# Performance work log

Measured on AMD Instinct MI355X. Metric: run time of the kernel, lower is better.

Reference implementation:

```python
import jax, jax.numpy as jnp
import numpy as np

B, L, E, D = 32, 1024, 512, 512  # batch, seq_len, input_size, per-direction hidden
SCALE = 1.4142135623730951  # rescale=True, highway_bias=0 -> sqrt(1+exp(0*2)) = sqrt(2)


def setup_inputs() -> dict:
    key = jax.random.key(0)
    ks = jax.random.split(key, 12)
    g = lambda k, shape, s: (jax.random.normal(k, shape, jnp.float32) * s)
    return {
        "seqs": jax.random.normal(ks[0], (B, L, E), jnp.float32),
        # layer 0: input E -> 2 dirs * 4 projections * D
        "W0": g(ks[1], (E, 8 * D), (1.0 / E) ** 0.5),
        "vf0": g(ks[2], (2, D), 0.1), "vr0": g(ks[3], (2, D), 0.1),
        "bf0": jnp.zeros((2, D), jnp.float32), "br0": jnp.zeros((2, D), jnp.float32),
        # layer 1: input 2D -> 2 dirs * 4 projections * D
        "W1": g(ks[4], (2 * D, 8 * D), (1.0 / (2 * D)) ** 0.5),
        "vf1": g(ks[5], (2, D), 0.1), "vr1": g(ks[6], (2, D), 0.1),
        "bf1": jnp.zeros((2, D), jnp.float32), "br1": jnp.zeros((2, D), jnp.float32),
        "lengths": jax.random.randint(ks[7], (B,), 1, L + 1, dtype=jnp.int32),
    }


def _sru_dir(u, vf, vr, bf, br, reverse):
    # u: (L, B, 4, D) -> h: (L, B, D), c_T: (B, D)
    def step(c, u_t):
        xt, fp, rp, xp = u_t[:, 0], u_t[:, 1], u_t[:, 2], u_t[:, 3]
        f = jax.nn.sigmoid(fp + vf * c + bf)
        c_new = f * c + (1.0 - f) * xt
        r = jax.nn.sigmoid(rp + vr * c + br)
        h = r * c_new + (1.0 - r) * xp * SCALE
        return c_new, h

    c0 = jnp.zeros((u.shape[1], u.shape[-1]), u.dtype)
    cT, hs = jax.lax.scan(step, c0, u, reverse=reverse)
    return hs, cT


def _sru_layer(x, W, vf, vr, bf, br):
    # x: (L, B, n_in)
    Lx, Bx = x.shape[0], x.shape[1]
    U = (x @ W).reshape(Lx, Bx, 2, 4, -1)  # dirs, (x_tilde, f, r, x_resid)
    h_f, c_f = _sru_dir(U[:, :, 0], vf[0], vr[0], bf[0], br[0], False)
    h_b, c_b = _sru_dir(U[:, :, 1], vf[1], vr[1], bf[1], br[1], True)
    return jnp.concatenate([h_f, h_b], -1), jnp.concatenate([c_f, c_b], -1)


def reference(seqs, W0, vf0, vr0, bf0, br0, W1, vf1, vr1, bf1, br1, lengths):
    x = jnp.transpose(seqs, (1, 0, 2))  # (L, B, E)
    out0, _ = _sru_layer(x, W0, vf0, vr0, bf0, br0)
    out1, c1 = _sru_layer(out0, W1, vf1, vr1, bf1, br1)
    # module returns (h[1], output.transpose(0,1)): layer-1 final cell state, (B,L,2D) outputs
    return c1, jnp.transpose(out1, (1, 0, 2))
```

## Files before the change

kernel.cpp:

```cpp
#include <hip/hip_runtime.h>
#include <cstdint>
#include <cstddef>

#define B_   32
#define L_   1024
#define D_   512
#define M_   (B_ * L_)
#define N8D  4096
#define SCALEF 1.4142135623730951f
#define LOG2E 1.4426950408889634f

typedef unsigned short u16;
typedef __bf16 bf16x8 __attribute__((ext_vector_type(8)));
typedef unsigned short u16x8 __attribute__((ext_vector_type(8)));
typedef unsigned short u16x4 __attribute__((ext_vector_type(4)));
typedef float f32x4 __attribute__((ext_vector_type(4)));

__device__ __forceinline__ float bf2f(u16 u) {
    union { unsigned int i; float f; } v; v.i = ((unsigned int)u) << 16; return v.f;
}
__device__ __forceinline__ u16 f2bf(float x) {
    union { float f; unsigned int i; } v; v.f = x;
    unsigned int r = (v.i + 0x7fffu + ((v.i >> 16) & 1u)) >> 16;
    return (u16)r;
}
__device__ __forceinline__ float sigmoid_fast(float z) {
    return __builtin_amdgcn_rcpf(1.0f + __builtin_amdgcn_exp2f(-LOG2E * z));
}

__device__ __forceinline__ void gl2lds16(const u16* g, u16* l) {
    __builtin_amdgcn_global_load_lds(
        (const __attribute__((address_space(1))) void*)g,
        (__attribute__((address_space(3))) void*)l, 16, 0, 0);
}

#define VMW(n) asm volatile("s_waitcnt vmcnt(" #n ")" ::: "memory")

__global__ __launch_bounds__(256) void f32_to_bf16(const float* __restrict__ in,
                                                   u16* __restrict__ out) {
    size_t i = ((size_t)blockIdx.x * 256 + threadIdx.x) * 8;
    f32x4 v0 = *(const f32x4*)(in + i);
    f32x4 v1 = *(const f32x4*)(in + i + 4);
    u16x8 o;
#pragma unroll
    for (int q = 0; q < 4; ++q) { o[q] = f2bf(v0[q]); o[4 + q] = f2bf(v1[q]); }
    *(u16x8*)(out + i) = o;
}

__global__ __launch_bounds__(256) void transpose_w(const float* __restrict__ in,
                                                   u16* __restrict__ out,
                                                   int R, int C) {
    __shared__ u16 tile[32][33];
    int bx = blockIdx.x * 32;
    int by = blockIdx.y * 32;
    int tx = threadIdx.x & 31;
    int ty = threadIdx.x >> 5;
#pragma unroll
    for (int i = 0; i < 32; i += 8)
        tile[ty + i][tx] = f2bf(in[(size_t)(by + ty + i) * C + bx + tx]);
    __syncthreads();
#pragma unroll
    for (int i = 0; i < 32; i += 8) {
        int n = bx + ty + i;
        int p = (n >> 11) * 2048 + ((n & 511) << 2) + ((n >> 9) & 3);
        out[(size_t)p * R + by + tx] = tile[tx][ty + i];
    }
}

__global__ __launch_bounds__(512, 2) void gemm256(const u16* __restrict__ A,
                                                  const u16* __restrict__ BT,
                                                  u16* __restrict__ U, int K) {
    extern __shared__ __align__(16) u16 lds[];
    const int t    = threadIdx.x;
    const int lane = t & 63;
    const int wave = t >> 6;
    const int wm   = wave >> 2;
    const int wn   = wave & 3;
    const int qm   = lane & 15;
    const int quad = lane >> 4;

    const int nwg = gridDim.x;
    const int wg  = blockIdx.x;
    const int swz = (wg & 7) * (nwg >> 3) + (wg >> 3);
    const int bn  = (swz & 15) << 8;
    const int bm  = (swz >> 4) << 8;

    const int P0   = t * 16;
    const int L0   = P0 ^ ((P0 >> 3) & 0x30);
    const int srow = L0 >> 6;
    const int scol = (L0 & 63) >> 1;
    const u16* Ag = A  + (size_t)(bm + srow) * K + scol;
    const u16* Bg = BT + (size_t)(bn + srow) * K + scol;
    const size_t g128 = (size_t)128 * K;
    u16* ldst = lds + t * 8;

    const int fxor  = (quad * 16) ^ ((qm & 6) << 3);
    const int aBase = (wm * 128 + qm) * 64 + fxor;
    const int bBase = (wn * 64  + qm) * 64 + fxor;
    const char* ldsc = (const char*)lds;

    f32x4 acc[8][4];
#pragma unroll
    for (int i = 0; i < 8; ++i)
#pragma unroll
        for (int j = 0; j < 4; ++j) acc[i][j] = (f32x4)(0.0f);

    bf16x8 aA[4], aB[4];
    bf16x8 bK0[4], bK1[4];

#define STG(op, tile, ks, buf) do {                                          \
        const u16* g_ = ((op) ? Bg : Ag) + (size_t)(tile) * 64 + (ks) * 32;  \
        u16* l_ = ldst + (buf) * 32768 + (op) * 16384 + (ks) * 8192;         \
        gl2lds16(g_, l_);                                                    \
        gl2lds16(g_ + g128, l_ + 4096);                                      \
    } while (0)

#define RD_A(dst, buf, ks, mh) do {                                          \
        _Pragma("unroll")                                                    \
        for (int mi = 0; mi < 4; ++mi)                                       \
            dst[mi] = *(const bf16x8*)(ldsc + ((buf) * 65536 + (ks) * 16384) \
                          + aBase + ((mh) * 64 + mi * 16) * 64);             \
    } while (0)

#define RD_B(dst, buf, ks) do {                                              \
        _Pragma("unroll")                                                    \
        for (int nj = 0; nj < 4; ++nj)                                       \
            dst[nj] = *(const bf16x8*)(ldsc + ((buf) * 65536 + 32768 +       \
                          (ks) * 16384) + bBase + nj * 16 * 64);             \
    } while (0)

#define MFMA16(mh, AU, BU) do {                                              \
        __builtin_amdgcn_s_barrier();                                        \
        asm volatile("s_waitcnt lgkmcnt(0)" ::: "memory");                   \
        __builtin_amdgcn_sched_barrier(0);                                   \
        __builtin_amdgcn_s_setprio(1);                                       \
        _Pragma("unroll")                                                    \
        for (int mi = 0; mi < 4; ++mi)                                       \
            _Pragma("unroll")                                                \
            for (int nj = 0; nj < 4; ++nj)                                   \
                acc[(mh) * 4 + mi][nj] = __builtin_amdgcn_mfma_f32_16x16x32_bf16( \
                    AU[mi], BU[nj], acc[(mh) * 4 + mi][nj], 0, 0, 0);        \
        __builtin_amdgcn_s_setprio(0);                                       \
    } while (0)

#define BARB __builtin_amdgcn_s_barrier()

    const int nt = K >> 6;

    STG(1, 0, 0, 0); STG(0, 0, 0, 0); STG(1, 0, 1, 0); STG(0, 0, 1, 0);
    VMW(4);
    STG(1, 1, 0, 1); STG(0, 1, 0, 1); STG(1, 1, 1, 1);
    VMW(6);
    __builtin_amdgcn_s_barrier();
    RD_A(aA, 0, 0, 0); RD_B(bK0, 0, 0);

    const int niter = (nt >> 1) - 1;
    for (int i = 0; i < niter; ++i) {
        const int tp1 = 2 * i + 1, tp2 = 2 * i + 2, tp3 = 2 * i + 3;
        STG(0, tp1, 1, 1); MFMA16(0, aA, bK0); RD_A(aB, 0, 0, 1); BARB;
        STG(1, tp2, 0, 0); MFMA16(1, aB, bK0); RD_A(aA, 0, 1, 0); RD_B(bK1, 0, 1); BARB;
        STG(0, tp2, 0, 0); MFMA16(0, aA, bK1); RD_A(aB, 0, 1, 1); BARB;
        STG(1, tp2, 1, 0); MFMA16(1, aB, bK1); VMW(6); RD_A(aA, 1, 0, 0); RD_B(bK0, 1, 0); BARB;
        STG(0, tp2, 1, 0); MFMA16(0, aA, bK0); RD_A(aB, 1, 0, 1); BARB;
        STG(1, tp3, 0, 1); MFMA16(1, aB, bK0); RD_A(aA, 1, 1, 0); RD_B(bK1, 1, 1); BARB;
        STG(0, tp3, 0, 1); MFMA16(0, aA, bK1); RD_A(aB, 1, 1, 1); BARB;
        STG(1, tp3, 1, 1); MFMA16(1, aB, bK1); VMW(6); RD_A(aA, 0, 0, 0); RD_B(bK0, 0, 0); BARB;
    }
    STG(0, nt - 1, 1, 1); MFMA16(0, aA, bK0); RD_A(aB, 0, 0, 1); BARB;
    MFMA16(1, aB, bK0); RD_A(aA, 0, 1, 0); RD_B(bK1, 0, 1); BARB;
    MFMA16(0, aA, bK1); RD_A(aB, 0, 1, 1); BARB;
    MFMA16(1, aB, bK1); VMW(4); RD_A(aA, 1, 0, 0); RD_B(bK0, 1, 0); BARB;
    MFMA16(0, aA, bK0); RD_A(aB, 1, 0, 1); BARB;
    MFMA16(1, aB, bK0); VMW(0); RD_A(aA, 1, 1, 0); RD_B(bK1, 1, 1); BARB;
    MFMA16(0, aA, bK1); RD_A(aB, 1, 1, 1); BARB;
    MFMA16(1, aB, bK1); BARB;

#undef BARB
#undef MFMA16
#undef RD_B
#undef RD_A
#undef STG

#pragma unroll
    for (int i8 = 0; i8 < 8; ++i8) {
        const int row0 = bm + wm * 128 + (i8 >> 2) * 64 + (i8 & 3) * 16 + quad * 4;
#pragma unroll
        for (int nj = 0; nj < 4; ++nj) {
            const int col = bn + wn * 64 + nj * 16 + qm;
#pragma unroll
            for (int r = 0; r < 4; ++r)
                U[(size_t)(row0 + r) * N8D + col] = f2bf(acc[i8][nj][r]);
        }
    }
}

template<bool OUT_F32>
__global__ __launch_bounds__(64) void sru_scan(const u16* __restrict__ U,
                                               const float* __restrict__ vf,
                                               const float* __restrict__ vr,
                                               const float* __restrict__ bfv,
                                               const float* __restrict__ brv,
                                               void* __restrict__ Hv,
                                               void* __restrict__ Cv) {
    constexpr int PF = 32;
    constexpr int NB = L_ / PF;

    int gid = blockIdx.x * blockDim.x + threadIdx.x;
    int d   = gid & (D_ - 1);
    int dir = (gid >> 9) & 1;
    int b   = gid >> 10;
    int ch  = dir * D_ + d;

    const float vf_v = vf[ch];
    const float vr_v = vr[ch];
    const float bf_v = bfv[ch];
    const float br_v = brv[ch];

    const ptrdiff_t ustep = dir ? -(ptrdiff_t)N8D : (ptrdiff_t)N8D;
    const ptrdiff_t hstep = dir ? -(ptrdiff_t)1024 : (ptrdiff_t)1024;
    const u16* p0 = U + (size_t)b * L_ * N8D + dir * 2048 + d * 4
                      + (dir ? (size_t)(L_ - 1) * N8D : 0);
    const size_t hstart = (size_t)b * L_ * 1024 + ch + (dir ? (size_t)(L_ - 1) * 1024 : 0);
    float* Hf = (float*)Hv + hstart;
    u16*   Hh = (u16*)Hv + hstart;

    float c = 0.0f;

    auto loadB = [&](u16x4 (&buf)[PF], int tb) {
        const u16* base = p0 + (ptrdiff_t)tb * PF * ustep;
#pragma unroll
        for (int i = 0; i < PF; ++i)
            buf[i] = *(const u16x4*)(base + (ptrdiff_t)i * ustep);
    };
    auto compStore = [&](u16x4 (&buf)[PF], int tb) {
        const ptrdiff_t hb = (ptrdiff_t)tb * PF * hstep;
#pragma unroll
        for (int i = 0; i < PF; ++i) {
            float xt = bf2f(buf[i][0]), fp = bf2f(buf[i][1]);
            float rp = bf2f(buf[i][2]), xp = bf2f(buf[i][3]);
            float f = sigmoid_fast(fp + vf_v * c + bf_v);
            float r = sigmoid_fast(rp + vr_v * c + br_v);
            c = f * (c - xt) + xt;
            float xs = xp * SCALEF;
            float h  = r * (c - xs) + xs;
            ptrdiff_t ho = hb + (ptrdiff_t)i * hstep;
            if (OUT_F32) Hf[ho] = h; else Hh[ho] = f2bf(h);
        }
    };

    u16x4 b0[PF], b1[PF];
    loadB(b0, 0);
    loadB(b1, 1);
    for (int t = 0; t < NB; t += 2) {
        compStore(b0, t);
        if (t + 2 < NB) loadB(b0, t + 2);
        compStore(b1, t + 1);
        if (t + 3 < NB) loadB(b1, t + 3);
    }

    if (OUT_F32) ((float*)Cv)[b * 1024 + ch] = c;
    else         ((u16*)Cv)[b * 1024 + ch]  = f2bf(c);
}

extern "C" void kernel_launch(void* const* d_in, const int* in_sizes, int n_in,
                              void* d_out, int out_size, void* d_ws, size_t ws_size,
                              hipStream_t stream) {
    (void)in_sizes; (void)n_in; (void)out_size; (void)ws_size;

    const float* seqs = (const float*)d_in[0];
    const float* W0   = (const float*)d_in[1];
    const float* vf0  = (const float*)d_in[2];
    const float* vr0  = (const float*)d_in[3];
    const float* bf0  = (const float*)d_in[4];
    const float* br0  = (const float*)d_in[5];
    const float* W1   = (const float*)d_in[6];
    const float* vf1  = (const float*)d_in[7];
    const float* vr1  = (const float*)d_in[8];
    const float* bf1  = (const float*)d_in[9];
    const float* br1  = (const float*)d_in[10];

    float* out = (float*)d_out;
    char* ws = (char*)d_ws;

    const size_t U_BYTES  = (size_t)M_ * N8D * 2;
    const size_t H_BYTES  = (size_t)M_ * 1024 * 2;
    const size_t W0T_B    = (size_t)4096 * 512 * 2;
    const size_t W1T_B    = (size_t)4096 * 1024 * 2;

    u16* U   = (u16*)(ws);
    u16* H0  = (u16*)(ws + U_BYTES);
    u16* S16 = H0;
    u16* W0T = (u16*)(ws + U_BYTES + H_BYTES);
    u16* W1T = (u16*)(ws + U_BYTES + H_BYTES + W0T_B);
    u16* Cd  = (u16*)(ws + U_BYTES + H_BYTES + W0T_B + W1T_B);

    f32_to_bf16<<<dim3(M_ * 512 / 8 / 256), 256, 0, stream>>>(seqs, S16);

    transpose_w<<<dim3(4096 / 32, 512 / 32), 256, 0, stream>>>(W0, W0T, 512, 4096);
    transpose_w<<<dim3(4096 / 32, 1024 / 32), 256, 0, stream>>>(W1, W1T, 1024, 4096);

    gemm256<<<dim3(2048), 512, 131072, stream>>>(S16, W0T, U, 512);
    sru_scan<false><<<dim3(512), 64, 0, stream>>>(U, vf0, vr0, bf0, br0, (void*)H0, (void*)Cd);

    gemm256<<<dim3(2048), 512, 131072, stream>>>(H0, W1T, U, 1024);
    sru_scan<true><<<dim3(512), 64, 0, stream>>>(U, vf1, vr1, bf1, br1,
                                                 (void*)(out + B_ * 1024), (void*)out);
}
```

Baseline: 774.5 us.

## Restructure GEMM main loop into per-k-slice phases with interleaved LDS waits

```diff
diff --git a/kernel.cpp b/kernel.cpp
--- a/kernel.cpp
+++ b/kernel.cpp
@@ -35,6 +35,8 @@
 }
 
 #define VMW(n) asm volatile("s_waitcnt vmcnt(" #n ")" ::: "memory")
+#define LGK(n) asm volatile("s_waitcnt lgkmcnt(" #n ")" ::: "memory")
+#define SB     __builtin_amdgcn_sched_barrier(0)
 
 __global__ __launch_bounds__(256) void f32_to_bf16(const float* __restrict__ in,
                                                    u16* __restrict__ out) {
@@ -105,81 +107,76 @@
 #pragma unroll
         for (int j = 0; j < 4; ++j) acc[i][j] = (f32x4)(0.0f);
 
-    bf16x8 aA[4], aB[4];
-    bf16x8 bK0[4], bK1[4];
-
-#define STG(op, tile, ks, buf) do {                                          \
+#define RD16(p) (*(const bf16x8*)(p))
+
+#define STGR(op, tile, ks, buf) do {                                         \
         const u16* g_ = ((op) ? Bg : Ag) + (size_t)(tile) * 64 + (ks) * 32;  \
         u16* l_ = ldst + (buf) * 32768 + (op) * 16384 + (ks) * 8192;         \
         gl2lds16(g_, l_);                                                    \
         gl2lds16(g_ + g128, l_ + 4096);                                      \
     } while (0)
 
-#define RD_A(dst, buf, ks, mh) do {                                          \
-        _Pragma("unroll")                                                    \
-        for (int mi = 0; mi < 4; ++mi)                                       \
-            dst[mi] = *(const bf16x8*)(ldsc + ((buf) * 65536 + (ks) * 16384) \
-                          + aBase + ((mh) * 64 + mi * 16) * 64);             \
-    } while (0)
-
-#define RD_B(dst, buf, ks) do {                                              \
+#define G4(g, av) do {                                                       \
         _Pragma("unroll")                                                    \
         for (int nj = 0; nj < 4; ++nj)                                       \
-            dst[nj] = *(const bf16x8*)(ldsc + ((buf) * 65536 + 32768 +       \
-                          (ks) * 16384) + bBase + nj * 16 * 64);             \
+            acc[g][nj] = __builtin_amdgcn_mfma_f32_16x16x32_bf16(            \
+                av, bb[nj], acc[g][nj], 0, 0, 0);                            \
     } while (0)
 
-#define MFMA16(mh, AU, BU) do {                                              \
-        __builtin_amdgcn_s_barrier();                                        \
-        asm volatile("s_waitcnt lgkmcnt(0)" ::: "memory");                   \
-        __builtin_amdgcn_sched_barrier(0);                                   \
+#define PH(buf, ks, stile, dostage, vmn, dobar) do {                         \
+        const char* As_ = ldsc + ((buf) * 32768 + (ks) * 8192) * 2;          \
+        const char* Bs_ = ldsc + ((buf) * 32768 + 16384 + (ks) * 8192) * 2;  \
+        bf16x8 bb[4], aa[8];                                                 \
+        bb[0] = RD16(Bs_ + bBase);        SB;                                \
+        bb[1] = RD16(Bs_ + bBase + 1024); SB;                                \
+        bb[2] = RD16(Bs_ + bBase + 2048); SB;                                \
+        bb[3] = RD16(Bs_ + bBase + 3072); SB;                                \
+        aa[0] = RD16(As_ + aBase);        SB;                                \
+        aa[1] = RD16(As_ + aBase + 1024); SB;                                \
+        aa[2] = RD16(As_ + aBase + 2048); SB;                                \
+        aa[3] = RD16(As_ + aBase + 3072); SB;                                \
+        aa[4] = RD16(As_ + aBase + 4096); SB;                                \
+        aa[5] = RD16(As_ + aBase + 5120); SB;                                \
+        aa[6] = RD16(As_ + aBase + 6144); SB;                                \
+        aa[7] = RD16(As_ + aBase + 7168); SB;                                \
+        if (dostage) { STGR(0, stile, ks, (buf) ^ 1);                        \
+                       STGR(1, stile, ks, (buf) ^ 1); }                      \
         __builtin_amdgcn_s_setprio(1);                                       \
-        _Pragma("unroll")                                                    \
-        for (int mi = 0; mi < 4; ++mi)                                       \
-            _Pragma("unroll")                                                \
-            for (int nj = 0; nj < 4; ++nj)                                   \
-                acc[(mh) * 4 + mi][nj] = __builtin_amdgcn_mfma_f32_16x16x32_bf16( \
-                    AU[mi], BU[nj], acc[(mh) * 4 + mi][nj], 0, 0, 0);        \
+        LGK(7); SB; G4(0, aa[0]); SB;                                        \
+        LGK(6); SB; G4(1, aa[1]); SB;                                        \
+        LGK(5); SB; G4(2, aa[2]); SB;                                        \
+        LGK(4); SB; G4(3, aa[3]); SB;                                        \
+        LGK(3); SB; G4(4, aa[4]); SB;                                        \
+        LGK(2); SB; G4(5, aa[5]); SB;                                        \
+        LGK(1); SB; G4(6, aa[6]); SB;                                        \
+        LGK(0); SB; G4(7, aa[7]); SB;                                        \
         __builtin_amdgcn_s_setprio(0);                                       \
+        if ((vmn) == 4) VMW(4); else if ((vmn) == 0) VMW(0);                 \
+        if (dobar) { SB; __builtin_amdgcn_s_barrier(); SB; }                 \
     } while (0)
 
-#define BARB __builtin_amdgcn_s_barrier()
-
     const int nt = K >> 6;
 
-    STG(1, 0, 0, 0); STG(0, 0, 0, 0); STG(1, 0, 1, 0); STG(0, 0, 1, 0);
+    STGR(0, 0, 0, 0); STGR(1, 0, 0, 0); STGR(0, 0, 1, 0); STGR(1, 0, 1, 0);
     VMW(4);
-    STG(1, 1, 0, 1); STG(0, 1, 0, 1); STG(1, 1, 1, 1);
-    VMW(6);
     __builtin_amdgcn_s_barrier();
-    RD_A(aA, 0, 0, 0); RD_B(bK0, 0, 0);
-
-    const int niter = (nt >> 1) - 1;
-    for (int i = 0; i < niter; ++i) {
-        const int tp1 = 2 * i + 1, tp2 = 2 * i + 2, tp3 = 2 * i + 3;
-        STG(0, tp1, 1, 1); MFMA16(0, aA, bK0); RD_A(aB, 0, 0, 1); BARB;
-        STG(1, tp2, 0, 0); MFMA16(1, aB, bK0); RD_A(aA, 0, 1, 0); RD_B(bK1, 0, 1); BARB;
-        STG(0, tp2, 0, 0); MFMA16(0, aA, bK1); RD_A(aB, 0, 1, 1); BARB;
-        STG(1, tp2, 1, 0); MFMA16(1, aB, bK1); VMW(6); RD_A(aA, 1, 0, 0); RD_B(bK0, 1, 0); BARB;
-        STG(0, tp2, 1, 0); MFMA16(0, aA, bK0); RD_A(aB, 1, 0, 1); BARB;
-        STG(1, tp3, 0, 1); MFMA16(1, aB, bK0); RD_A(aA, 1, 1, 0); RD_B(bK1, 1, 1); BARB;
-        STG(0, tp3, 0, 1); MFMA16(0, aA, bK1); RD_A(aB, 1, 1, 1); BARB;
-        STG(1, tp3, 1, 1); MFMA16(1, aB, bK1); VMW(6); RD_A(aA, 0, 0, 0); RD_B(bK0, 0, 0); BARB;
+
+    for (int i = 0; i < (nt >> 1) - 1; ++i) {
+        const int t2 = 2 * i;
+        PH(0, 0, t2 + 1, 1, 4, 1);
+        PH(0, 1, t2 + 1, 1, 4, 1);
+        PH(1, 0, t2 + 2, 1, 4, 1);
+        PH(1, 1, t2 + 2, 1, 4, 1);
     }
-    STG(0, nt - 1, 1, 1); MFMA16(0, aA, bK0); RD_A(aB, 0, 0, 1); BARB;
-    MFMA16(1, aB, bK0); RD_A(aA, 0, 1, 0); RD_B(bK1, 0, 1); BARB;
-    MFMA16(0, aA, bK1); RD_A(aB, 0, 1, 1); BARB;
-    MFMA16(1, aB, bK1); VMW(4); RD_A(aA, 1, 0, 0); RD_B(bK0, 1, 0); BARB;
-    MFMA16(0, aA, bK0); RD_A(aB, 1, 0, 1); BARB;
-    MFMA16(1, aB, bK0); VMW(0); RD_A(aA, 1, 1, 0); RD_B(bK1, 1, 1); BARB;
-    MFMA16(0, aA, bK1); RD_A(aB, 1, 1, 1); BARB;
-    MFMA16(1, aB, bK1); BARB;
-
-#undef BARB
-#undef MFMA16
-#undef RD_B
-#undef RD_A
-#undef STG
+    PH(0, 0, nt - 1, 1, 4, 1);
+    PH(0, 1, nt - 1, 1, 4, 1);
+    PH(1, 0, 0, 0, 0, 1);
+    PH(1, 1, 0, 0, -1, 0);
+
+#undef PH
+#undef G4
+#undef STGR
+#undef RD16
 
 #pragma unroll
     for (int i8 = 0; i8 < 8; ++i8) {
```

Result: slower. 818.6 us (+5.7%).
